# Performance work log

Measured on AMD Instinct MI355X. Metric: run time of the kernel, lower is better.

Reference implementation:

```python
import jax, jax.numpy as jnp
import numpy as np

N_NODES = 100000
N_EDGES = 1600000
N_GRAPHS = 512
HID = 192
EPS = 1e-5


def setup_inputs() -> dict:
    key = jax.random.key(0)
    ks = jax.random.split(key, 16)
    x = jax.random.normal(ks[0], (N_NODES, 1), dtype=jnp.float32)
    edge_index = jax.random.randint(ks[1], (2, N_EDGES), 0, N_NODES, dtype=jnp.int64)
    batch = jnp.sort(jax.random.randint(ks[2], (N_NODES,), 0, N_GRAPHS, dtype=jnp.int64))
    def lin(k, fi, fo):
        # torch nn.Linear default init: U(-1/sqrt(fi), 1/sqrt(fi))
        b = 1.0 / np.sqrt(fi)
        return jax.random.uniform(k, (fi, fo), jnp.float32, -b, b)
    return {
        "x": x, "edge_index": edge_index, "batch": batch,
        "W1": lin(ks[3], 1, HID), "b1": jnp.zeros((HID,), jnp.float32),
        "g1": jnp.ones((HID,), jnp.float32), "be1": jnp.zeros((HID,), jnp.float32), "a1": jnp.ones((HID,), jnp.float32),
        "W2": lin(ks[4], HID, HID), "b2": jnp.zeros((HID,), jnp.float32),
        "g2": jnp.ones((HID,), jnp.float32), "be2": jnp.zeros((HID,), jnp.float32), "a2": jnp.ones((HID,), jnp.float32),
        "Wc1": lin(ks[5], HID, HID // 2), "bc1": jax.random.uniform(ks[6], (HID // 2,), jnp.float32, -1/np.sqrt(HID), 1/np.sqrt(HID)),
        "Wc2": lin(ks[7], HID // 2, 4), "bc2": jax.random.uniform(ks[8], (4,), jnp.float32, -1/np.sqrt(HID // 2), 1/np.sqrt(HID // 2)),
    }


def gcn_conv(x, W, b, row, col, n):
    # PyG GCNConv: h = xW; add self-loops; norm = d^-1/2[src] * d^-1/2[dst]; scatter-add to dst; + bias
    h = x @ W
    sl = jnp.arange(n, dtype=row.dtype)
    r = jnp.concatenate([row, sl])
    c = jnp.concatenate([col, sl])
    deg = jax.ops.segment_sum(jnp.ones_like(c, dtype=h.dtype), c, num_segments=n)
    dinv = jnp.where(deg > 0, jax.lax.rsqrt(deg), 0.0)
    norm = dinv[r] * dinv[c]                      # [E+N]
    msg = h[r] * norm[:, None]                    # [E+N, HID] dominant gather
    return jax.ops.segment_sum(msg, c, num_segments=n) + b


def graph_norm(x, batch, gamma, beta, alpha, g):
    cnt = jax.ops.segment_sum(jnp.ones((x.shape[0],), x.dtype), batch, num_segments=g)
    cnt = jnp.maximum(cnt, 1.0)[:, None]
    mean = jax.ops.segment_sum(x, batch, num_segments=g) / cnt
    out = x - alpha * mean[batch]
    var = jax.ops.segment_sum(out * out, batch, num_segments=g) / cnt
    out = out * jax.lax.rsqrt(var + EPS)[batch]
    return gamma * out + beta


def reference(x, edge_index, batch, W1, b1, g1, be1, a1, W2, b2, g2, be2, a2, Wc1, bc1, Wc2, bc2):
    n = x.shape[0]
    row, col = edge_index[0], edge_index[1]
    h = gcn_conv(x, W1, b1, row, col, n)
    h = jax.nn.relu(graph_norm(h, batch, g1, be1, a1, N_GRAPHS))
    h = gcn_conv(h, W2, b2, row, col, n)
    h = jax.nn.relu(graph_norm(h, batch, g2, be2, a2, N_GRAPHS))
    # global mean pool (dropout is identity in eval mode)
    cnt = jnp.maximum(jax.ops.segment_sum(jnp.ones((n,), h.dtype), batch, num_segments=N_GRAPHS), 1.0)
    pooled = jax.ops.segment_sum(h, batch, num_segments=N_GRAPHS) / cnt[:, None]
    z = jax.nn.relu(pooled @ Wc1 + bc1)
    return z @ Wc2 + bc2
```

## Files before the change

### kernel.cpp

```cpp
#include <hip/hip_runtime.h>
#include <hip/hip_bf16.h>
#include <hip/hip_fp16.h>

#define N_NODES 100000
#define N_PAD 100032
#define N_EDGES 1600000
#define N_GRAPHS 512
#define HID 192
#define EPSV 1e-5f

using f16x8 = __attribute__((ext_vector_type(8))) _Float16;
using f16x4 = __attribute__((ext_vector_type(4))) _Float16;
using f32x4 = __attribute__((ext_vector_type(4))) float;

__global__ void k_count(const int* __restrict__ col, int* __restrict__ cnt) {
    int e = blockIdx.x * blockDim.x + threadIdx.x;
    if (e < N_EDGES) atomicAdd(&cnt[col[e]], 1);
}

__global__ void k_misc(const float* __restrict__ W2, _Float16* __restrict__ W2h,
                       const int* __restrict__ batch, int* __restrict__ gstart) {
    int id = blockIdx.x * blockDim.x + threadIdx.x;
    if (id < HID * HID) W2h[id] = (_Float16)W2[id];
    int g = id - HID * HID;
    if (g >= 0 && g <= N_GRAPHS) {
        if (g == N_GRAPHS) { gstart[g] = N_NODES; return; }
        int lo = 0, hi = N_NODES;
        while (lo < hi) { int mid = (lo + hi) >> 1; if (batch[mid] < g) lo = mid + 1; else hi = mid; }
        gstart[g] = lo;
    }
}

__global__ void k_scan_partial(const int* __restrict__ cnt, int* __restrict__ bsum) {
    __shared__ int sd[256];
    int base = blockIdx.x * 1024;
    int t = threadIdx.x;
    int s = 0;
    for (int j = 0; j < 4; ++j) {
        int i = base + j * 256 + t;
        if (i < N_NODES) s += cnt[i];
    }
    sd[t] = s; __syncthreads();
    for (int off = 128; off > 0; off >>= 1) {
        if (t < off) sd[t] += sd[t + off];
        __syncthreads();
    }
    if (t == 0) bsum[blockIdx.x] = sd[0];
}

__global__ void k_scan_bsum(int* __restrict__ bsum, int nb, int* __restrict__ row_ptr) {
    if (threadIdx.x == 0 && blockIdx.x == 0) {
        int run = 0;
        for (int b = 0; b < nb; ++b) { int v = bsum[b]; bsum[b] = run; run += v; }
        row_ptr[N_NODES] = run;
    }
}

__global__ void k_scan_final(const int* __restrict__ cnt, const int* __restrict__ bsum,
                             int* __restrict__ row_ptr, int* __restrict__ cursor,
                             float* __restrict__ dinv, const float* __restrict__ x,
                             float* __restrict__ xp) {
    __shared__ int sd[256];
    int base = blockIdx.x * 1024;
    int t = threadIdx.x;
    int idx0 = base + t * 4;
    int c[4]; int tot = 0;
    for (int j = 0; j < 4; ++j) {
        int i = idx0 + j;
        c[j] = (i < N_NODES) ? cnt[i] : 0;
        tot += c[j];
    }
    sd[t] = tot; __syncthreads();
    for (int off = 1; off < 256; off <<= 1) {
        int v = (t >= off) ? sd[t - off] : 0;
        __syncthreads();
        sd[t] += v;
        __syncthreads();
    }
    int excl = sd[t] - tot + bsum[blockIdx.x];
    for (int j = 0; j < 4; ++j) {
        int i = idx0 + j;
        if (i < N_NODES) {
            row_ptr[i] = excl;
            cursor[i] = excl;
            float dv = rsqrtf((float)(c[j] + 1));
            dinv[i] = dv;
            xp[i] = x[i] * dv;
            excl += c[j];
        }
    }
}

#define FILL_PASSES 8
#define FILL_RANGE (N_NODES / FILL_PASSES)
__global__ void __launch_bounds__(256) k_fill(const int* __restrict__ row,
                                              const int* __restrict__ col,
                                              int* __restrict__ cursor,
                                              int* __restrict__ csr_src) {
    int tid = blockIdx.x * blockDim.x + threadIdx.x;
    int stride = gridDim.x * blockDim.x;
    for (int p = 0; p < FILL_PASSES; ++p) {
        int lo = p * FILL_RANGE;
        int hi = (p == FILL_PASSES - 1) ? N_NODES : lo + FILL_RANGE;
        for (int e = tid; e < N_EDGES; e += stride) {
            int c = col[e];
            if (c >= lo && c < hi) {
                int pos = atomicAdd(&cursor[c], 1);
                csr_src[pos] = row[e];
            }
        }
    }
}

__global__ void k_layer1(const float* __restrict__ x, const float* __restrict__ xp,
                         const int* __restrict__ batch,
                         const int* __restrict__ row_ptr, const int* __restrict__ csr_src,
                         const float* __restrict__ dinv, float4* __restrict__ node_info) {
    int v = blockIdx.x * blockDim.x + threadIdx.x;
    if (v >= N_NODES) return;
    int e0 = row_ptr[v], e1 = row_ptr[v + 1];
    float acc = 0.f;
    for (int base = e0; base < e1; base += 16) {
        int src[16]; float xv[16];
#pragma unroll
        for (int j = 0; j < 16; ++j) { int e = base + j; src[j] = csr_src[(e < e1) ? e : e0]; }
#pragma unroll
        for (int j = 0; j < 16; ++j) { xv[j] = xp[src[j]]; }
#pragma unroll
        for (int j = 0; j < 16; ++j) { acc += (base + j < e1) ? xv[j] : 0.f; }
    }
    float dv = dinv[v];
    float u = dv * acc + x[v] * dv * dv;
    node_info[v] = make_float4(u, dv, __int_as_float((int)batch[v]), 0.f);
}

__global__ void __launch_bounds__(64) k_stats1(const float4* __restrict__ node_info,
                                               const int* __restrict__ gstart,
                                               float* __restrict__ sum_u, float* __restrict__ sum_u2) {
    int g = blockIdx.x, t = threadIdx.x;
    int i0 = gstart[g], i1 = gstart[g + 1];
    float s = 0.f, s2 = 0.f;
    for (int i = i0 + t; i < i1; i += 64) { float u = node_info[i].x; s += u; s2 += u * u; }
#pragma unroll
    for (int off = 32; off; off >>= 1) { s += __shfl_down(s, off); s2 += __shfl_down(s2, off); }
    if (t == 0) { sum_u[g] = s; sum_u2[g] = s2; }
}

__global__ void k_ab(const float* __restrict__ sum_u, const float* __restrict__ sum_u2,
                     const int* __restrict__ gstart,
                     const float* __restrict__ W1, const float* __restrict__ b1,
                     const float* __restrict__ g1, const float* __restrict__ be1,
                     const float* __restrict__ a1,
                     float* __restrict__ A, float* __restrict__ B) {
    int id = blockIdx.x * blockDim.x + threadIdx.x;
    if (id >= N_GRAPHS * HID) return;
    int g = id / HID, f = id % HID;
    float cntf = fmaxf((float)(gstart[g + 1] - gstart[g]), 1.f);
    float m = sum_u[g] / cntf;
    float es2 = sum_u2[g] / cntf;
    float w = W1[f], bb = b1[f], al = a1[f];
    float c2 = bb * (1.f - al);
    float d = al * m;
    float eud2 = es2 - 2.f * d * m + d * d;
    float var = w * w * eud2 + 2.f * w * c2 * (m - d) + c2 * c2;
    float rs = rsqrtf(var + EPSV);
    float gam = g1[f];
    A[id] = gam * rs * w;
    B[id] = gam * rs * (c2 - w * d) + be1[f];
}

__global__ void __launch_bounds__(256) k_x1(const float4* __restrict__ node_info,
                                            const float* __restrict__ A,
                                            const float* __restrict__ B,
                                            _Float16* __restrict__ X1p) {
    int wid = threadIdx.x >> 6;
    int lane = threadIdx.x & 63;
    int v = blockIdx.x * 4 + wid;
    if (v >= N_NODES) return;
    float4 ni = node_info[v];
    float u = ni.x, dv = ni.y;
    int g = __float_as_int(ni.z);
    int c4 = (lane < 48 ? lane : 47) * 4;
    float4 Av = *(const float4*)(A + g * HID + c4);
    float4 Bv = *(const float4*)(B + g * HID + c4);
    f16x4 o;
    o[0] = (_Float16)(fmaxf(fmaf(Av.x, u, Bv.x), 0.f) * dv);
    o[1] = (_Float16)(fmaxf(fmaf(Av.y, u, Bv.y), 0.f) * dv);
    o[2] = (_Float16)(fmaxf(fmaf(Av.z, u, Bv.z), 0.f) * dv);
    o[3] = (_Float16)(fmaxf(fmaf(Av.w, u, Bv.w), 0.f) * dv);
    if (lane < 48) *(f16x4*)(X1p + (size_t)v * HID + c4) = o;
}

#define CH 8
__global__ void __launch_bounds__(256) k_conv2(const _Float16* __restrict__ X1p,
                                               const float* __restrict__ dinv,
                                               const int* __restrict__ row_ptr,
                                               const int* __restrict__ csr_src,
                                               _Float16* __restrict__ aggh) {
    int wid = threadIdx.x >> 6;
    int lane = threadIdx.x & 63;
    int v = blockIdx.x * 4 + wid;
    if (v >= N_NODES) return;
    int c4 = (lane < 48 ? lane : 47) * 4;
    float dv = dinv[v];
    f16x4 sv = *(const f16x4*)(X1p + (size_t)v * HID + c4);
    float a0 = (float)sv[0], a1 = (float)sv[1], a2 = (float)sv[2], a3 = (float)sv[3];
    int e0 = row_ptr[v], e1 = row_ptr[v + 1];
    for (int b = e0; b < e1; b += CH) {
        int src[CH]; float wgt[CH];
#pragma unroll
        for (int j = 0; j < CH; ++j) {
            int e = b + j;
            src[j] = csr_src[(e < e1) ? e : e0];
            wgt[j] = (e < e1) ? 1.f : 0.f;
        }
        f16x4 rv[CH];
#pragma unroll
        for (int j = 0; j < CH; ++j)
            rv[j] = *(const f16x4*)(X1p + (size_t)src[j] * HID + c4);
#pragma unroll
        for (int j = 0; j < CH; ++j) {
            a0 = fmaf(wgt[j], (float)rv[j][0], a0);
            a1 = fmaf(wgt[j], (float)rv[j][1], a1);
            a2 = fmaf(wgt[j], (float)rv[j][2], a2);
            a3 = fmaf(wgt[j], (float)rv[j][3], a3);
        }
    }
    if (lane < 48) {
        f16x4 o;
        o[0] = (_Float16)(a0 * dv);
        o[1] = (_Float16)(a1 * dv);
        o[2] = (_Float16)(a2 * dv);
        o[3] = (_Float16)(a3 * dv);
        *(f16x4*)(aggh + (size_t)v * HID + c4) = o;
    }
}

#define BM 64
__global__ void __launch_bounds__(256) k_gemm(const _Float16* __restrict__ A,
                                              const _Float16* __restrict__ W,
                                              const float* __restrict__ b2,
                                              _Float16* __restrict__ H) {
    __shared__ _Float16 a_lds[BM * HID];
    int t = threadIdx.x;
    int wid = t >> 6, lane = t & 63;
    int row0 = blockIdx.x * BM;
    const char* Ablk = (const char*)(A + (size_t)row0 * HID);
#pragma unroll
    for (int it = 0; it < 6; ++it) {
        int bo = (it * 256 + t) * 16;
        int r = bo / 384;
        int swz = bo ^ ((r & 7) << 4);
        *(float4*)((char*)a_lds + swz) = *(const float4*)(Ablk + bo);
    }
    int n0 = wid * 48;
    int bn = n0 + (lane & 15);
    int bk0 = (lane >> 4) << 3;
    f16x8 bfr[6][3];
#pragma unroll
    for (int kc = 0; kc < 6; ++kc)
#pragma unroll
        for (int nt = 0; nt < 3; ++nt) {
            const _Float16* src = W + (size_t)(kc * 32 + bk0) * HID + bn + nt * 16;
            f16x8 v;
#pragma unroll
            for (int j = 0; j < 8; ++j) v[j] = src[(size_t)j * HID];
            bfr[kc][nt] = v;
        }
    __syncthreads();
    f32x4 acc[4][3];
#pragma unroll
    for (int mt = 0; mt < 4; ++mt)
#pragma unroll
        for (int nt = 0; nt < 3; ++nt) acc[mt][nt] = (f32x4){0.f, 0.f, 0.f, 0.f};
    int ar = lane & 15;
#pragma unroll
    for (int mt = 0; mt < 4; ++mt) {
        int r = mt * 16 + ar;
        int rbase = r * 384;
        int sw = (r & 7) << 4;
#pragma unroll
        for (int kc = 0; kc < 6; ++kc) {
            int bo = (rbase + (kc * 32 + bk0) * 2) ^ sw;
            f16x8 a = *(const f16x8*)((const char*)a_lds + bo);
            acc[mt][0] = __builtin_amdgcn_mfma_f32_16x16x32_f16(a, bfr[kc][0], acc[mt][0], 0, 0, 0);
            acc[mt][1] = __builtin_amdgcn_mfma_f32_16x16x32_f16(a, bfr[kc][1], acc[mt][1], 0, 0, 0);
            acc[mt][2] = __builtin_amdgcn_mfma_f32_16x16x32_f16(a, bfr[kc][2], acc[mt][2], 0, 0, 0);
        }
    }
    int cn = lane & 15;
    int rb = (lane >> 4) * 4;
    float bias[3];
#pragma unroll
    for (int nt = 0; nt < 3; ++nt) bias[nt] = b2[n0 + nt * 16 + cn];
#pragma unroll
    for (int mt = 0; mt < 4; ++mt)
#pragma unroll
        for (int nt = 0; nt < 3; ++nt) {
            int col = n0 + nt * 16 + cn;
#pragma unroll
            for (int r = 0; r < 4; ++r) {
                int grow = row0 + mt * 16 + rb + r;
                if (grow < N_NODES)
                    H[(size_t)grow * HID + col] = (_Float16)(acc[mt][nt][r] + bias[nt]);
            }
        }
}

__global__ void __launch_bounds__(192) k_stats2(const _Float16* __restrict__ h,
                                                const int* __restrict__ batch,
                                                float* __restrict__ sums,
                                                float* __restrict__ sumsq) {
    int f = threadIdx.x;
    int r0 = blockIdx.x * 64;
    int r1 = min(r0 + 64, N_NODES);
    int g = batch[r0];
    float s = 0.f, s2 = 0.f;
    int i = r0;
    for (; i + 4 <= r1; i += 4) {
        int g0 = batch[i], g3 = batch[i + 3];
        float v0 = (float)h[(size_t)(i + 0) * HID + f];
        float v1 = (float)h[(size_t)(i + 1) * HID + f];
        float v2 = (float)h[(size_t)(i + 2) * HID + f];
        float v3 = (float)h[(size_t)(i + 3) * HID + f];
        if (g0 == g && g3 == g) {
            s += v0 + v1 + v2; s += v3;
            s2 += v0 * v0 + v1 * v1; s2 += v2 * v2 + v3 * v3;
        } else {
            float vv[4] = {v0, v1, v2, v3};
            for (int j = 0; j < 4; ++j) {
                int gi = batch[i + j];
                if (gi != g) {
                    atomicAdd(&sums[g * HID + f], s);
                    atomicAdd(&sumsq[g * HID + f], s2);
                    s = 0.f; s2 = 0.f; g = gi;
                }
                s += vv[j]; s2 += vv[j] * vv[j];
            }
        }
    }
    for (; i < r1; ++i) {
        int gi = batch[i];
        float v = (float)h[(size_t)i * HID + f];
        if (gi != g) {
            atomicAdd(&sums[g * HID + f], s);
            atomicAdd(&sumsq[g * HID + f], s2);
            s = 0.f; s2 = 0.f; g = gi;
        }
        s += v; s2 += v * v;
    }
    atomicAdd(&sums[g * HID + f], s);
    atomicAdd(&sumsq[g * HID + f], s2);
}

__global__ void k_cd(const float* __restrict__ sums, const float* __restrict__ sumsq,
                     const int* __restrict__ gstart,
                     const float* __restrict__ g2, const float* __restrict__ be2,
                     const float* __restrict__ a2,
                     float* __restrict__ C, float* __restrict__ D) {
    int id = blockIdx.x * blockDim.x + threadIdx.x;
    if (id >= N_GRAPHS * HID) return;
    int g = id / HID, f = id % HID;
    float cntf = fmaxf((float)(gstart[g + 1] - gstart[g]), 1.f);
    float mh = sums[id] / cntf;
    float msq = sumsq[id] / cntf;
    float al = a2[f];
    float var = msq - 2.f * al * mh * mh + al * al * mh * mh;
    float Cv = g2[f] * rsqrtf(var + EPSV);
    C[id] = Cv;
    D[id] = be2[f] - Cv * al * mh;
}

__global__ void __launch_bounds__(192) k_pool(const _Float16* __restrict__ h,
                                              const int* __restrict__ batch,
                                              const float* __restrict__ C,
                                              const float* __restrict__ D,
                                              float* __restrict__ pooled) {
    int f = threadIdx.x;
    int r0 = blockIdx.x * 64;
    int r1 = min(r0 + 64, N_NODES);
    int g = batch[r0];
    float Cg = C[g * HID + f], Dg = D[g * HID + f];
    float s = 0.f;
    int i = r0;
    for (; i + 4 <= r1; i += 4) {
        int g0 = batch[i], g3 = batch[i + 3];
        float v0 = (float)h[(size_t)(i + 0) * HID + f];
        float v1 = (float)h[(size_t)(i + 1) * HID + f];
        float v2 = (float)h[(size_t)(i + 2) * HID + f];
        float v3 = (float)h[(size_t)(i + 3) * HID + f];
        if (g0 == g && g3 == g) {
            s += fmaxf(fmaf(Cg, v0, Dg), 0.f) + fmaxf(fmaf(Cg, v1, Dg), 0.f);
            s += fmaxf(fmaf(Cg, v2, Dg), 0.f) + fmaxf(fmaf(Cg, v3, Dg), 0.f);
        } else {
            float vv[4] = {v0, v1, v2, v3};
            for (int j = 0; j < 4; ++j) {
                int gi = batch[i + j];
                if (gi != g) {
                    atomicAdd(&pooled[g * HID + f], s);
                    s = 0.f; g = gi;
                    Cg = C[g * HID + f]; Dg = D[g * HID + f];
                }
                s += fmaxf(fmaf(Cg, vv[j], Dg), 0.f);
            }
        }
    }
    for (; i < r1; ++i) {
        int gi = batch[i];
        float v = (float)h[(size_t)i * HID + f];
        if (gi != g) {
            atomicAdd(&pooled[g * HID + f], s);
            s = 0.f; g = gi;
            Cg = C[g * HID + f]; Dg = D[g * HID + f];
        }
        s += fmaxf(fmaf(Cg, v, Dg), 0.f);
    }
    atomicAdd(&pooled[g * HID + f], s);
}

__global__ void __launch_bounds__(128) k_mlp(const float* __restrict__ pooled,
                                             const int* __restrict__ gstart,
                                             const float* __restrict__ Wc1,
                                             const float* __restrict__ bc1,
                                             const float* __restrict__ Wc2,
                                             const float* __restrict__ bc2,
                                             float* __restrict__ out) {
    __shared__ float p[HID];
    __shared__ float z[96];
    int g = blockIdx.x, t = threadIdx.x;
    float inv = 1.f / fmaxf((float)(gstart[g + 1] - gstart[g]), 1.f);
    for (int i = t; i < HID; i += 128) p[i] = pooled[g * HID + i] * inv;
    __syncthreads();
    if (t < 96) {
        float acc = bc1[t];
        for (int k = 0; k < HID; ++k) acc += p[k] * Wc1[k * 96 + t];
        z[t] = fmaxf(acc, 0.f);
    }
    __syncthreads();
    if (t < 4) {
        float acc = bc2[t];
        for (int j = 0; j < 96; ++j) acc += z[j] * Wc2[j * 4 + t];
        out[g * 4 + t] = acc;
    }
}

extern "C" void kernel_launch(void* const* d_in, const int* in_sizes, int n_in,
                              void* d_out, int out_size, void* d_ws, size_t ws_size,
                              hipStream_t stream) {
    const float* x   = (const float*)d_in[0];
    const int* eidx  = (const int*)d_in[1];
    const int* batch = (const int*)d_in[2];
    const float* W1  = (const float*)d_in[3];
    const float* b1  = (const float*)d_in[4];
    const float* g1  = (const float*)d_in[5];
    const float* be1 = (const float*)d_in[6];
    const float* a1  = (const float*)d_in[7];
    const float* W2  = (const float*)d_in[8];
    const float* b2  = (const float*)d_in[9];
    const float* g2  = (const float*)d_in[10];
    const float* be2 = (const float*)d_in[11];
    const float* a2  = (const float*)d_in[12];
    const float* Wc1 = (const float*)d_in[13];
    const float* bc1 = (const float*)d_in[14];
    const float* Wc2 = (const float*)d_in[15];
    const float* bc2 = (const float*)d_in[16];
    const int* row = eidx;
    const int* col = eidx + N_EDGES;
    float* out = (float*)d_out;

    char* ws = (char*)d_ws;
    size_t off = 0;
    auto alloc = [&](size_t bytes) -> char* {
        char* p = ws + off;
        off = (off + bytes + 255) & ~(size_t)255;
        return p;
    };
    int*   cnt     = (int*)  alloc(N_NODES * 4);
    float* sums2   = (float*)alloc(N_GRAPHS * HID * 4);
    float* sumsq2  = (float*)alloc(N_GRAPHS * HID * 4);
    float* pooled  = (float*)alloc(N_GRAPHS * HID * 4);
    size_t zbytes  = off;
    int*   bsum    = (int*)  alloc(128 * 4);
    int*   row_ptr = (int*)  alloc((N_NODES + 1) * 4);
    int*   cursor  = (int*)  alloc(N_NODES * 4);
    int*   csr_src = (int*)  alloc(N_EDGES * 4);
    float* dinv    = (float*)alloc(N_NODES * 4);
    float* xp      = (float*)alloc(N_NODES * 4);
    float4* node_info = (float4*)alloc((size_t)N_NODES * 16);
    float* sum_u   = (float*)alloc(N_GRAPHS * 4);
    float* sum_u2  = (float*)alloc(N_GRAPHS * 4);
    float* Atab    = (float*)alloc(N_GRAPHS * HID * 4);
    float* Btab    = (float*)alloc(N_GRAPHS * HID * 4);
    float* Ctab    = (float*)alloc(N_GRAPHS * HID * 4);
    float* Dtab    = (float*)alloc(N_GRAPHS * HID * 4);
    int*   gstart  = (int*)  alloc((N_GRAPHS + 1) * 4);
    _Float16* X1p  = (_Float16*)alloc((size_t)N_NODES * HID * 2);
    _Float16* aggh = (_Float16*)alloc((size_t)N_PAD * HID * 2);
    _Float16* h2   = (_Float16*)alloc((size_t)N_NODES * HID * 2);
    _Float16* W2h  = (_Float16*)alloc((size_t)HID * HID * 2);

    hipMemsetAsync(ws, 0, zbytes, stream);
    k_misc<<<(HID * HID + N_GRAPHS + 1 + 255) / 256, 256, 0, stream>>>(W2, W2h, batch, gstart);
    k_count<<<(N_EDGES + 255) / 256, 256, 0, stream>>>(col, cnt);
    int PB = (N_NODES + 1023) / 1024;
    k_scan_partial<<<PB, 256, 0, stream>>>(cnt, bsum);
    k_scan_bsum<<<1, 64, 0, stream>>>(bsum, PB, row_ptr);
    k_scan_final<<<PB, 256, 0, stream>>>(cnt, bsum, row_ptr, cursor, dinv, x, xp);
    k_fill<<<2048, 256, 0, stream>>>(row, col, cursor, csr_src);
    k_layer1<<<(N_NODES + 255) / 256, 256, 0, stream>>>(x, xp, batch, row_ptr, csr_src, dinv, node_info);
    k_stats1<<<N_GRAPHS, 64, 0, stream>>>(node_info, gstart, sum_u, sum_u2);
    k_ab<<<(N_GRAPHS * HID + 255) / 256, 256, 0, stream>>>(sum_u, sum_u2, gstart,
                                                           W1, b1, g1, be1, a1, Atab, Btab);
    k_x1<<<(N_NODES + 3) / 4, 256, 0, stream>>>(node_info, Atab, Btab, X1p);
    k_conv2<<<(N_NODES + 3) / 4, 256, 0, stream>>>(X1p, dinv, row_ptr, csr_src, aggh);
    k_gemm<<<(N_NODES + BM - 1) / BM, 256, 0, stream>>>(aggh, W2h, b2, h2);
    int SB = (N_NODES + 63) / 64;
    k_stats2<<<SB, 192, 0, stream>>>(h2, batch, sums2, sumsq2);
    k_cd<<<(N_GRAPHS * HID + 255) / 256, 256, 0, stream>>>(sums2, sumsq2, gstart,
                                                           g2, be2, a2, Ctab, Dtab);
    k_pool<<<SB, 192, 0, stream>>>(h2, batch, Ctab, Dtab, pooled);
    k_mlp<<<N_GRAPHS, 128, 0, stream>>>(pooled, gstart, Wc1, bc1, Wc2, bc2, out);
}
```

Baseline: 376.5 us.

## Fuse scan/stats kernels and precompute byte offsets for conv2 gather

Removes the single-thread bsum scan kernel by having each scan_final block reduce preceding block sums itself. Merges the per-graph stats and affine-coefficient kernels into one 192-thread block per graph. Also writes a precomputed byte-offset array during CSR fill, so the layer-2 gather uses 32-bit unsigned address arithmetic instead of 64-bit multiplies. This cuts two launches and some address math, at the cost of an extra 6.4MB array write in k_fill.

```diff
diff --git a/kernel.cpp b/kernel.cpp
--- a/kernel.cpp
+++ b/kernel.cpp
@@ -48,21 +48,24 @@
     if (t == 0) bsum[blockIdx.x] = sd[0];
 }
 
-__global__ void k_scan_bsum(int* __restrict__ bsum, int nb, int* __restrict__ row_ptr) {
-    if (threadIdx.x == 0 && blockIdx.x == 0) {
-        int run = 0;
-        for (int b = 0; b < nb; ++b) { int v = bsum[b]; bsum[b] = run; run += v; }
-        row_ptr[N_NODES] = run;
-    }
-}
-
 __global__ void k_scan_final(const int* __restrict__ cnt, const int* __restrict__ bsum,
-                             int* __restrict__ row_ptr, int* __restrict__ cursor,
+                             int nb, int* __restrict__ row_ptr, int* __restrict__ cursor,
                              float* __restrict__ dinv, const float* __restrict__ x,
                              float* __restrict__ xp) {
     __shared__ int sd[256];
-    int base = blockIdx.x * 1024;
+    __shared__ int s_off;
+    int bid = blockIdx.x;
     int t = threadIdx.x;
+    int part = 0;
+    for (int i = t; i < bid; i += 256) part += bsum[i];
+    sd[t] = part; __syncthreads();
+    for (int off = 128; off > 0; off >>= 1) {
+        if (t < off) sd[t] += sd[t + off];
+        __syncthreads();
+    }
+    if (t == 0) s_off = sd[0];
+    __syncthreads();
+    int base = bid * 1024;
     int idx0 = base + t * 4;
     int c[4]; int tot = 0;
     for (int j = 0; j < 4; ++j) {
@@ -77,7 +80,7 @@
         sd[t] += v;
         __syncthreads();
     }
-    int excl = sd[t] - tot + bsum[blockIdx.x];
+    int excl = sd[t] - tot + s_off;
     for (int j = 0; j < 4; ++j) {
         int i = idx0 + j;
         if (i < N_NODES) {
@@ -89,6 +92,7 @@
             excl += c[j];
         }
     }
+    if (bid == nb - 1 && t == 255) row_ptr[N_NODES] = excl;
 }
 
 #define FILL_PASSES 8
@@ -96,7 +100,8 @@
 __global__ void __launch_bounds__(256) k_fill(const int* __restrict__ row,
                                               const int* __restrict__ col,
                                               int* __restrict__ cursor,
-                                              int* __restrict__ csr_src) {
+                                              int* __restrict__ csr_src,
+                                              int* __restrict__ csr_off) {
     int tid = blockIdx.x * blockDim.x + threadIdx.x;
     int stride = gridDim.x * blockDim.x;
     for (int p = 0; p < FILL_PASSES; ++p) {
@@ -105,8 +110,10 @@
         for (int e = tid; e < N_EDGES; e += stride) {
             int c = col[e];
             if (c >= lo && c < hi) {
+                int r = row[e];
                 int pos = atomicAdd(&cursor[c], 1);
-                csr_src[pos] = row[e];
+                csr_src[pos] = r;
+                csr_off[pos] = r * (HID * 2);
             }
         }
     }
@@ -134,30 +141,28 @@
     node_info[v] = make_float4(u, dv, __int_as_float((int)batch[v]), 0.f);
 }
 
-__global__ void __launch_bounds__(64) k_stats1(const float4* __restrict__ node_info,
-                                               const int* __restrict__ gstart,
-                                               float* __restrict__ sum_u, float* __restrict__ sum_u2) {
+__global__ void __launch_bounds__(192) k_stats_ab(const float4* __restrict__ node_info,
+                                                  const int* __restrict__ gstart,
+                                                  const float* __restrict__ W1, const float* __restrict__ b1,
+                                                  const float* __restrict__ g1, const float* __restrict__ be1,
+                                                  const float* __restrict__ a1,
+                                                  float* __restrict__ A, float* __restrict__ B) {
+    __shared__ float sd[192], sd2[192];
     int g = blockIdx.x, t = threadIdx.x;
     int i0 = gstart[g], i1 = gstart[g + 1];
     float s = 0.f, s2 = 0.f;
-    for (int i = i0 + t; i < i1; i += 64) { float u = node_info[i].x; s += u; s2 += u * u; }
-#pragma unroll
-    for (int off = 32; off; off >>= 1) { s += __shfl_down(s, off); s2 += __shfl_down(s2, off); }
-    if (t == 0) { sum_u[g] = s; sum_u2[g] = s2; }
-}
-
-__global__ void k_ab(const float* __restrict__ sum_u, const float* __restrict__ sum_u2,
-                     const int* __restrict__ gstart,
-                     const float* __restrict__ W1, const float* __restrict__ b1,
-                     const float* __restrict__ g1, const float* __restrict__ be1,
-                     const float* __restrict__ a1,
-                     float* __restrict__ A, float* __restrict__ B) {
-    int id = blockIdx.x * blockDim.x + threadIdx.x;
-    if (id >= N_GRAPHS * HID) return;
-    int g = id / HID, f = id % HID;
-    float cntf = fmaxf((float)(gstart[g + 1] - gstart[g]), 1.f);
-    float m = sum_u[g] / cntf;
-    float es2 = sum_u2[g] / cntf;
+    for (int i = i0 + t; i < i1; i += 192) { float u = node_info[i].x; s += u; s2 += u * u; }
+    sd[t] = s; sd2[t] = s2; __syncthreads();
+    for (int off = 96; off >= 3; off >>= 1) {
+        if (t < off) { sd[t] += sd[t + off]; sd2[t] += sd2[t + off]; }
+        __syncthreads();
+    }
+    float sum_u = sd[0] + sd[1] + sd[2];
+    float sum_u2 = sd2[0] + sd2[1] + sd2[2];
+    float cntf = fmaxf((float)(i1 - i0), 1.f);
+    float m = sum_u / cntf;
+    float es2 = sum_u2 / cntf;
+    int f = t;
     float w = W1[f], bb = b1[f], al = a1[f];
     float c2 = bb * (1.f - al);
     float d = al * m;
@@ -165,8 +170,8 @@
     float var = w * w * eud2 + 2.f * w * c2 * (m - d) + c2 * c2;
     float rs = rsqrtf(var + EPSV);
     float gam = g1[f];
-    A[id] = gam * rs * w;
-    B[id] = gam * rs * (c2 - w * d) + be1[f];
+    A[g * HID + f] = gam * rs * w;
+    B[g * HID + f] = gam * rs * (c2 - w * d) + be1[f];
 }
 
 __global__ void __launch_bounds__(256) k_x1(const float4* __restrict__ node_info,
@@ -195,29 +200,30 @@
 __global__ void __launch_bounds__(256) k_conv2(const _Float16* __restrict__ X1p,
                                                const float* __restrict__ dinv,
                                                const int* __restrict__ row_ptr,
-                                               const int* __restrict__ csr_src,
+                                               const int* __restrict__ csr_off,
                                                _Float16* __restrict__ aggh) {
     int wid = threadIdx.x >> 6;
     int lane = threadIdx.x & 63;
     int v = blockIdx.x * 4 + wid;
     if (v >= N_NODES) return;
-    int c4 = (lane < 48 ? lane : 47) * 4;
+    unsigned c8 = (unsigned)(lane < 48 ? lane : 47) * 8u;
+    const char* Xb = (const char*)X1p;
     float dv = dinv[v];
-    f16x4 sv = *(const f16x4*)(X1p + (size_t)v * HID + c4);
+    f16x4 sv = *(const f16x4*)(Xb + (unsigned)v * (HID * 2) + c8);
     float a0 = (float)sv[0], a1 = (float)sv[1], a2 = (float)sv[2], a3 = (float)sv[3];
     int e0 = row_ptr[v], e1 = row_ptr[v + 1];
     for (int b = e0; b < e1; b += CH) {
-        int src[CH]; float wgt[CH];
+        unsigned off[CH]; float wgt[CH];
 #pragma unroll
         for (int j = 0; j < CH; ++j) {
             int e = b + j;
-            src[j] = csr_src[(e < e1) ? e : e0];
+            off[j] = (unsigned)csr_off[(e < e1) ? e : e0] + c8;
             wgt[j] = (e < e1) ? 1.f : 0.f;
         }
         f16x4 rv[CH];
 #pragma unroll
         for (int j = 0; j < CH; ++j)
-            rv[j] = *(const f16x4*)(X1p + (size_t)src[j] * HID + c4);
+            rv[j] = *(const f16x4*)(Xb + off[j]);
 #pragma unroll
         for (int j = 0; j < CH; ++j) {
             a0 = fmaf(wgt[j], (float)rv[j][0], a0);
@@ -232,7 +238,7 @@
         o[1] = (_Float16)(a1 * dv);
         o[2] = (_Float16)(a2 * dv);
         o[3] = (_Float16)(a3 * dv);
-        *(f16x4*)(aggh + (size_t)v * HID + c4) = o;
+        *(f16x4*)((char*)aggh + (unsigned)v * (HID * 2) + c8) = o;
     }
 }
 
@@ -484,11 +490,10 @@
     int*   row_ptr = (int*)  alloc((N_NODES + 1) * 4);
     int*   cursor  = (int*)  alloc(N_NODES * 4);
     int*   csr_src = (int*)  alloc(N_EDGES * 4);
+    int*   csr_off = (int*)  alloc(N_EDGES * 4);
     float* dinv    = (float*)alloc(N_NODES * 4);
     float* xp      = (float*)alloc(N_NODES * 4);
     float4* node_info = (float4*)alloc((size_t)N_NODES * 16);
-    float* sum_u   = (float*)alloc(N_GRAPHS * 4);
-    float* sum_u2  = (float*)alloc(N_GRAPHS * 4);
     float* Atab    = (float*)alloc(N_GRAPHS * HID * 4);
     float* Btab    = (float*)alloc(N_GRAPHS * HID * 4);
     float* Ctab    = (float*)alloc(N_GRAPHS * HID * 4);
@@ -504,15 +509,12 @@
     k_count<<<(N_EDGES + 255) / 256, 256, 0, stream>>>(col, cnt);
     int PB = (N_NODES + 1023) / 1024;
     k_scan_partial<<<PB, 256, 0, stream>>>(cnt, bsum);
-    k_scan_bsum<<<1, 64, 0, stream>>>(bsum, PB, row_ptr);
-    k_scan_final<<<PB, 256, 0, stream>>>(cnt, bsum, row_ptr, cursor, dinv, x, xp);
-    k_fill<<<2048, 256, 0, stream>>>(row, col, cursor, csr_src);
+    k_scan_final<<<PB, 256, 0, stream>>>(cnt, bsum, PB, row_ptr, cursor, dinv, x, xp);
+    k_fill<<<2048, 256, 0, stream>>>(row, col, cursor, csr_src, csr_off);
     k_layer1<<<(N_NODES + 255) / 256, 256, 0, stream>>>(x, xp, batch, row_ptr, csr_src, dinv, node_info);
-    k_stats1<<<N_GRAPHS, 64, 0, stream>>>(node_info, gstart, sum_u, sum_u2);
-    k_ab<<<(N_GRAPHS * HID + 255) / 256, 256, 0, stream>>>(sum_u, sum_u2, gstart,
-                                                           W1, b1, g1, be1, a1, Atab, Btab);
+    k_stats_ab<<<N_GRAPHS, 192, 0, stream>>>(node_info, gstart, W1, b1, g1, be1, a1, Atab, Btab);
     k_x1<<<(N_NODES + 3) / 4, 256, 0, stream>>>(node_info, Atab, Btab, X1p);
-    k_conv2<<<(N_NODES + 3) / 4, 256, 0, stream>>>(X1p, dinv, row_ptr, csr_src, aggh);
+    k_conv2<<<(N_NODES + 3) / 4, 256, 0, stream>>>(X1p, dinv, row_ptr, csr_off, aggh);
     k_gemm<<<(N_NODES + BM - 1) / BM, 256, 0, stream>>>(aggh, W2h, b2, h2);
     int SB = (N_NODES + 63) / 64;
     k_stats2<<<SB, 192, 0, stream>>>(h2, batch, sums2, sumsq2);
```

New measurement: 372.1 us. About the same (-1.2%).
